# Kernel optimization log

Hardware: AMD Instinct MI355X
Metric: run time of the kernel (lower is better)

## Reference

```python
import jax, jax.numpy as jnp
import numpy as np

B, N, H, D = 4, 2048, 16, 64
FEATS = H * D  # 1024; module scales scores by sqrt(feats), not sqrt(head_dim)


def setup_inputs() -> dict:
    key = jax.random.key(0)
    ks = jax.random.split(key, 9)
    s = 1.0 / np.sqrt(D)
    return {
        "x": jax.random.normal(ks[0], (B, N, H, D), dtype=jnp.float32),
        "Wq": jax.random.uniform(ks[1], (H, D, D), jnp.float32, -s, s),
        "bq": jax.random.uniform(ks[2], (H, D), jnp.float32, -s, s),
        "Wk": jax.random.uniform(ks[3], (H, D, D), jnp.float32, -s, s),
        "bk": jax.random.uniform(ks[4], (H, D), jnp.float32, -s, s),
        "Wv": jax.random.uniform(ks[5], (H, D, D), jnp.float32, -s, s),
        "bv": jax.random.uniform(ks[6], (H, D), jnp.float32, -s, s),
        "Wo": jax.random.uniform(ks[7], (H, D, D), jnp.float32, -s, s),
        "bo": jax.random.uniform(ks[8], (H, D), jnp.float32, -s, s),
    }


def reference(x, Wq, bq, Wk, bk, Wv, bv, Wo, bo):
    # per-head linears as one batched einsum: [b,n,h,d] x [h,d,o] -> [b,n,h,o]
    q = jnp.einsum("bnhd,hdo->bnho", x, Wq) + bq
    k = jnp.einsum("bnhd,hdo->bnho", x, Wk) + bk
    v = jnp.einsum("bnhd,hdo->bnho", x, Wv) + bv
    sqrt_d = jnp.asarray(FEATS, x.dtype) ** 0.5  # sqrt(feats) per original code
    # scores: [b,h,i,j]
    score = jax.nn.softmax(jnp.einsum("bihf,bjhf->bhij", q, k) / sqrt_d, axis=-1)
    attn = jnp.einsum("bhij,bjhf->bihf", score, v)  # [b,n,h,d]
    out = jnp.einsum("bnhd,hdo->bnho", attn, Wo) + bo
    return out
```

## Files before the change

### kernel.cpp

```cpp
#include <hip/hip_runtime.h>

#define Bsz  4
#define Nseq 2048
#define Hn   16
#define Dh   64
#define BH   (Bsz*Hn)
#define NT64 (Nseq/64)
#define NT32 (Nseq/32)

#define AS1 __attribute__((address_space(1)))
#define AS3 __attribute__((address_space(3)))

typedef __attribute__((ext_vector_type(8))) short bf16x8;
typedef __attribute__((ext_vector_type(16))) float f32x16;
typedef __attribute__((ext_vector_type(4))) float f32x4;
typedef __attribute__((ext_vector_type(2))) float f32x2;
typedef __attribute__((ext_vector_type(4))) unsigned short u16x4;

#define MFMA32 __builtin_amdgcn_mfma_f32_32x32x16_bf16

static __device__ __forceinline__ unsigned short f2bf(float f) {
    unsigned u = __float_as_uint(f);
    u = (u + 0x7fffu + ((u >> 16) & 1u)) >> 16;
    return (unsigned short)u;
}
static __device__ __forceinline__ float bf2f(unsigned short s) {
    return __uint_as_float((unsigned)s << 16);
}
static __device__ __forceinline__ unsigned cvt_pk_bf16(float lo, float hi) {
    unsigned r;
    asm("v_cvt_pk_bf16_f32 %0, %1, %2" : "=v"(r) : "v"(lo), "v"(hi));
    return r;
}
static __device__ __forceinline__ void swap32(unsigned &a, unsigned &b) {
    asm("v_permlane32_swap_b32 %0, %1" : "+v"(a), "+v"(b));
}
static __device__ __forceinline__ float exp2v(float x) {
    float r;
    asm("v_exp_f32 %0, %1" : "=v"(r) : "v"(x));
    return r;
}
static __device__ __forceinline__ f32x2 pk_add(f32x2 a, f32x2 b) {
    f32x2 d;
    asm("v_pk_add_f32 %0, %1, %2" : "=v"(d) : "v"(a), "v"(b));
    return d;
}

__global__ __launch_bounds__(256) void wprep_kernel(
    const float* __restrict__ Wq, const float* __restrict__ Wk,
    const float* __restrict__ Wv,
    unsigned short* __restrict__ gWtH, unsigned short* __restrict__ gWtL)
{
    __shared__ float ws[64][65];
    const int mh = blockIdx.x;
    const int m = mh >> 4, h = mh & 15;
    const int tid = threadIdx.x;
    const float* W = (m == 0 ? Wq : (m == 1 ? Wk : Wv)) + h * 4096;

    for (int c = tid; c < 1024; c += 256) {
        int row = c >> 4, col = (c & 15) * 4;
        *(f32x4*)&ws[row][col] = *(const f32x4*)&W[row * 64 + col];
    }
    __syncthreads();

    const int o = tid >> 2, dblk = (tid & 3) * 16;
    size_t base = ((size_t)mh * 64 + o) * 64 + dblk;
#pragma unroll
    for (int i4 = 0; i4 < 4; ++i4) {
        u16x4 vh, vl;
#pragma unroll
        for (int j = 0; j < 4; ++j) {
            float v = ws[dblk + i4 * 4 + j][o];
            unsigned short hh = f2bf(v);
            vh[j] = hh;
            vl[j] = f2bf(v - bf2f(hh));
        }
        *(u16x4*)&gWtH[base + i4 * 4] = vh;
        *(u16x4*)&gWtL[base + i4 * 4] = vl;
    }
}

__global__ __launch_bounds__(256) void proj_kernel(
    const float* __restrict__ x,
    const unsigned short* __restrict__ gWtH, const unsigned short* __restrict__ gWtL,
    const float* __restrict__ bq, const float* __restrict__ bk,
    const float* __restrict__ bv,
    unsigned short* __restrict__ gQ, unsigned short* __restrict__ gK,
    unsigned short* __restrict__ gVt)
{
    __shared__ unsigned short st[64][72];

    const int bh = blockIdx.x, h = bh & (Hn - 1), b = bh >> 4;
    const int n0 = blockIdx.y * 64;
    const int tid = threadIdx.x;
    const int w = tid >> 6, lane = tid & 63, l31 = lane & 31, l5 = lane >> 5;
    const int qi = w >> 1, oj = w & 1;

    const int nrow = n0 + qi * 32 + l31;
    const float* xrow = x + (((size_t)b * Nseq + nrow) * Hn + h) * Dh;

    bf16x8 xh[4], xl[4];
#pragma unroll
    for (int ks = 0; ks < 4; ++ks) {
        f32x4 v0 = *(const f32x4*)&xrow[ks * 16 + l5 * 8];
        f32x4 v1 = *(const f32x4*)&xrow[ks * 16 + l5 * 8 + 4];
#pragma unroll
        for (int e = 0; e < 4; ++e) {
            unsigned short h0 = f2bf(v0[e]);
            xh[ks][e] = (short)h0;
            xl[ks][e] = (short)f2bf(v0[e] - bf2f(h0));
            unsigned short h1 = f2bf(v1[e]);
            xh[ks][4 + e] = (short)h1;
            xl[ks][4 + e] = (short)f2bf(v1[e] - bf2f(h1));
        }
    }

    const int o = oj * 32 + l31;

    f32x16 acc[3] = {};
#pragma unroll
    for (int m = 0; m < 3; ++m) {
        const unsigned short* WH = gWtH + (((size_t)m * 16 + h) * 64 + o) * 64;
        const unsigned short* WL = gWtL + (((size_t)m * 16 + h) * 64 + o) * 64;
#pragma unroll
        for (int ks = 0; ks < 4; ++ks) {
            bf16x8 wh = *(const bf16x8*)&WH[ks * 16 + l5 * 8];
            bf16x8 wl = *(const bf16x8*)&WL[ks * 16 + l5 * 8];
            if (m < 2) {
                acc[m] = MFMA32(xh[ks], wh, acc[m], 0, 0, 0);
                acc[m] = MFMA32(xl[ks], wh, acc[m], 0, 0, 0);
                acc[m] = MFMA32(xh[ks], wl, acc[m], 0, 0, 0);
            } else {
                acc[2] = MFMA32(wh, xh[ks], acc[2], 0, 0, 0);
                acc[2] = MFMA32(wl, xh[ks], acc[2], 0, 0, 0);
                acc[2] = MFMA32(wh, xl[ks], acc[2], 0, 0, 0);
            }
        }
    }

    const size_t gbase = (size_t)bh * Nseq + n0;

    {
        float bias = bq[h * 64 + o];
#pragma unroll
        for (int r = 0; r < 16; ++r) {
            int nl = (r & 3) + 8 * (r >> 2) + 4 * l5;
            st[qi * 32 + nl][o] = f2bf((acc[0][r] + bias) * 0.0450842200f);
        }
    }
    __syncthreads();
#pragma unroll
    for (int i = 0; i < 2; ++i) {
        int c = i * 256 + tid;
        int row = c >> 3, ch = c & 7;
        bf16x8 v = *(const bf16x8*)&st[row][ch * 8];
        *(bf16x8*)&gQ[(gbase + row) * Dh + ch * 8] = v;
    }
    __syncthreads();

    {
        float bias = bk[h * 64 + o];
#pragma unroll
        for (int r = 0; r < 16; ++r) {
            int nl = (r & 3) + 8 * (r >> 2) + 4 * l5;
            st[qi * 32 + nl][o] = f2bf(acc[1][r] + bias);
        }
    }
    __syncthreads();
#pragma unroll
    for (int i = 0; i < 2; ++i) {
        int c = i * 256 + tid;
        int row = c >> 3, ch = c & 7;
        bf16x8 v = *(const bf16x8*)&st[row][ch * 8];
        *(bf16x8*)&gK[(gbase + row) * Dh + ((ch ^ (row & 7)) * 8)] = v;
    }
    __syncthreads();

    {
#pragma unroll
        for (int r = 0; r < 16; ++r) {
            int ol = (r & 3) + 8 * (r >> 2) + 4 * l5;
            int ov = oj * 32 + ol;
            st[ov][qi * 32 + l31] = f2bf(acc[2][r] + bv[h * 64 + ov]);
        }
    }
    __syncthreads();
#pragma unroll
    for (int i = 0; i < 2; ++i) {
        int c = i * 256 + tid;
        int orow = c >> 3, ch = c & 7;
        int tile = ch >> 2, c4 = ch & 3;
        bf16x8 v = *(const bf16x8*)&st[orow][ch * 8];
        *(bf16x8*)&gVt[((size_t)(bh * NT32 + (n0 >> 5) + tile)) * 2048 +
                       orow * 32 + ((c4 ^ ((orow >> 2) & 3)) * 8)] = v;
    }
}

__global__ __launch_bounds__(256, 4) void flash_kernel(
    const unsigned short* __restrict__ gQ,
    const unsigned short* __restrict__ gK,
    const unsigned short* __restrict__ gVt,
    const float* __restrict__ Wo, const float* __restrict__ bo,
    float* __restrict__ out)
{
    __shared__ unsigned short kbuf[2][4096];
    __shared__ unsigned short vbuf[2][4096];

    const int bh = blockIdx.x, h = bh & (Hn - 1), b = bh >> 4;
    const int tid = threadIdx.x;
    const int w = tid >> 6, lane = tid & 63;
    const int l31 = lane & 31, l5 = lane >> 5;
    const int qrow = blockIdx.y * 128 + w * 32 + l31;

    bf16x8 qf[4];
#pragma unroll
    for (int kk = 0; kk < 4; ++kk)
        qf[kk] = *(const bf16x8*)&gQ[((size_t)bh * Nseq + qrow) * Dh + kk * 16 + l5 * 8];

    const unsigned short* kbase[4];
#pragma unroll
    for (int kk = 0; kk < 4; ++kk)
        kbase[kk] = &kbuf[0][l31 * 64 + (((kk * 2 + l5) ^ (l31 & 7)) * 8)];
    const unsigned short* vbase[2];
#pragma unroll
    for (int ks = 0; ks < 2; ++ks)
        vbase[ks] = &vbuf[0][l31 * 32 + (((ks * 2 + l5) ^ ((l31 >> 2) & 3)) * 8)];

    float z0 = 0.f;
    asm volatile("" : "+v"(z0));
    f32x16 zc = {z0, z0, z0, z0, z0, z0, z0, z0, z0, z0, z0, z0, z0, z0, z0, z0};

    f32x16 acc[2] = {};
    float l = 0.f;

    auto stage = [&](int t, int bufi) {
        const unsigned short* ks = gK + ((size_t)bh * Nseq + (size_t)t * 64) * Dh;
        const unsigned short* vs = gVt + ((size_t)(bh * NT32 + 2 * t)) * 2048;
#pragma unroll
        for (int i = 0; i < 2; ++i) {
            int off = w * 1024 + i * 512 + lane * 8;
            __builtin_amdgcn_global_load_lds((const AS1 void*)(ks + off),
                                             (AS3 void*)(&kbuf[bufi][w * 1024 + i * 512]), 16, 0, 0);
            __builtin_amdgcn_global_load_lds((const AS1 void*)(vs + off),
                                             (AS3 void*)(&vbuf[bufi][w * 1024 + i * 512]), 16, 0, 0);
        }
    };

    auto soft_pv = [&](f32x16& s, const int sub, const int buf) {
#pragma unroll
        for (int r = 0; r < 16; ++r) s[r] = exp2v(s[r]);
        f32x2* sp = (f32x2*)&s;
        f32x2 u0 = pk_add(sp[0], sp[1]), u1 = pk_add(sp[2], sp[3]);
        f32x2 u2 = pk_add(sp[4], sp[5]), u3 = pk_add(sp[6], sp[7]);
        u0 = pk_add(u0, u1); u2 = pk_add(u2, u3);
        u0 = pk_add(u0, u2);
        l += u0[0] + u0[1];
#pragma unroll
        for (int ks = 0; ks < 2; ++ks) {
            const int b0 = 8 * ks;
            unsigned x0 = cvt_pk_bf16(s[b0 + 0], s[b0 + 1]);
            unsigned x1 = cvt_pk_bf16(s[b0 + 2], s[b0 + 3]);
            unsigned y0 = cvt_pk_bf16(s[b0 + 4], s[b0 + 5]);
            unsigned y1 = cvt_pk_bf16(s[b0 + 6], s[b0 + 7]);
            swap32(x0, y0);
            swap32(x1, y1);
            bf16x8 pf;
            ((unsigned*)&pf)[0] = x0; ((unsigned*)&pf)[1] = x1;
            ((unsigned*)&pf)[2] = y0; ((unsigned*)&pf)[3] = y1;
            __builtin_amdgcn_s_setprio(1);
#pragma unroll
            for (int dt = 0; dt < 2; ++dt) {
                bf16x8 vf = *(const bf16x8*)(vbase[ks] + dt * 1024 + sub * 2048 + buf * 4096);
                acc[dt] = MFMA32(vf, pf, acc[dt], 0, 0, 0);
            }
            __builtin_amdgcn_s_setprio(0);
        }
    };

    auto window = [&](const int buf) {
        f32x16 sA, sB;
        __builtin_amdgcn_s_setprio(1);
        {
            bf16x8 kf = *(const bf16x8*)(kbase[0] + buf * 4096);
            sA = MFMA32(kf, qf[0], zc, 0, 0, 0);
            kf = *(const bf16x8*)(kbase[1] + buf * 4096);
            sA = MFMA32(kf, qf[1], sA, 0, 0, 0);
            kf = *(const bf16x8*)(kbase[2] + buf * 4096);
            sA = MFMA32(kf, qf[2], sA, 0, 0, 0);
            kf = *(const bf16x8*)(kbase[3] + buf * 4096);
            sA = MFMA32(kf, qf[3], sA, 0, 0, 0);
            kf = *(const bf16x8*)(kbase[0] + 2048 + buf * 4096);
            sB = MFMA32(kf, qf[0], zc, 0, 0, 0);
            kf = *(const bf16x8*)(kbase[1] + 2048 + buf * 4096);
            sB = MFMA32(kf, qf[1], sB, 0, 0, 0);
            kf = *(const bf16x8*)(kbase[2] + 2048 + buf * 4096);
            sB = MFMA32(kf, qf[2], sB, 0, 0, 0);
            kf = *(const bf16x8*)(kbase[3] + 2048 + buf * 4096);
            sB = MFMA32(kf, qf[3], sB, 0, 0, 0);
        }
        __builtin_amdgcn_s_setprio(0);
        soft_pv(sA, 0, buf);
        soft_pv(sB, 1, buf);
    };

    stage(0, 0);

#pragma unroll 1
    for (int t2 = 0; t2 < NT64; t2 += 2) {
        __syncthreads();
        stage(t2 + 1, 1);
        window(0);
        __syncthreads();
        if (t2 + 2 < NT64) stage(t2 + 2, 0);
        window(1);
    }

    __syncthreads();
    {
        unsigned short* wl = &kbuf[0][0];
        for (int c = tid; c < 512; c += 256) {
            int o = c >> 3, c8 = c & 7;
            int cc = ((c8 ^ (o & 7)) * 8);
#pragma unroll
            for (int jj = 0; jj < 4; ++jj) wl[o * 64 + cc + jj]     = f2bf(Wo[(h * 64 + c8 * 8 + jj) * 64 + o]);
#pragma unroll
            for (int jj = 0; jj < 4; ++jj) wl[o * 64 + cc + 4 + jj] = f2bf(Wo[(h * 64 + c8 * 8 + 4 + jj) * 64 + o]);
        }
    }
    __syncthreads();

    l += __shfl_xor(l, 32);
    float inv = 1.f / l;
#pragma unroll
    for (int dt = 0; dt < 2; ++dt)
#pragma unroll
        for (int r = 0; r < 16; ++r) acc[dt][r] *= inv;

    f32x16 oc[2] = {};
#pragma unroll
    for (int kk = 0; kk < 4; ++kk) {
        const int dt = kk >> 1;
        const int b0 = 8 * (kk & 1);
        unsigned x0 = cvt_pk_bf16(acc[dt][b0 + 0], acc[dt][b0 + 1]);
        unsigned x1 = cvt_pk_bf16(acc[dt][b0 + 2], acc[dt][b0 + 3]);
        unsigned y0 = cvt_pk_bf16(acc[dt][b0 + 4], acc[dt][b0 + 5]);
        unsigned y1 = cvt_pk_bf16(acc[dt][b0 + 6], acc[dt][b0 + 7]);
        swap32(x0, y0);
        swap32(x1, y1);
        bf16x8 af;
        ((unsigned*)&af)[0] = x0; ((unsigned*)&af)[1] = x1;
        ((unsigned*)&af)[2] = y0; ((unsigned*)&af)[3] = y1;
#pragma unroll
        for (int ot = 0; ot < 2; ++ot) {
            bf16x8 wf = *(const bf16x8*)(kbase[kk] + ot * 2048);
            oc[ot] = MFMA32(wf, af, oc[ot], 0, 0, 0);
        }
    }

    float* obase = out + (((size_t)b * Nseq + qrow) * Hn + h) * Dh;
#pragma unroll
    for (int ot = 0; ot < 2; ++ot)
#pragma unroll
        for (int rq = 0; rq < 4; ++rq) {
            int o = ot * 32 + rq * 8 + l5 * 4;
            f32x4 bb = *(const f32x4*)&bo[h * 64 + o];
            f32x4 vv;
            vv[0] = oc[ot][rq * 4 + 0] + bb[0];
            vv[1] = oc[ot][rq * 4 + 1] + bb[1];
            vv[2] = oc[ot][rq * 4 + 2] + bb[2];
            vv[3] = oc[ot][rq * 4 + 3] + bb[3];
            *(f32x4*)&obase[o] = vv;
        }
}

extern "C" void kernel_launch(void* const* d_in, const int* in_sizes, int n_in,
                              void* d_out, int out_size, void* d_ws, size_t ws_size,
                              hipStream_t stream) {
    const float* x  = (const float*)d_in[0];
    const float* Wq = (const float*)d_in[1];
    const float* bq = (const float*)d_in[2];
    const float* Wk = (const float*)d_in[3];
    const float* bk = (const float*)d_in[4];
    const float* Wv = (const float*)d_in[5];
    const float* bv = (const float*)d_in[6];
    const float* Wo = (const float*)d_in[7];
    const float* bo = (const float*)d_in[8];
    float* out = (float*)d_out;

    unsigned short* gQ   = (unsigned short*)d_ws;
    unsigned short* gK   = gQ + (size_t)BH * Nseq * Dh;
    unsigned short* gVt  = gK + (size_t)BH * Nseq * Dh;
    unsigned short* gWtH = gVt + (size_t)BH * Nseq * Dh;
    unsigned short* gWtL = gWtH + (size_t)3 * 16 * 64 * 64;

    wprep_kernel<<<48, 256, 0, stream>>>(Wq, Wk, Wv, gWtH, gWtL);
    proj_kernel<<<dim3(BH, Nseq / 64), 256, 0, stream>>>(x, gWtH, gWtL, bq, bk, bv, gQ, gK, gVt);
    flash_kernel<<<dim3(BH, Nseq / 128), 256, 0, stream>>>(gQ, gK, gVt, Wo, bo, out);
}
```

Measured before the change: 130.3 us.

## Software-pipeline QK of next tile with softmax/PV of current tile

Restructures the flash attention main loop so the QK^T MFMAs for tile t+1 are issued alongside the exp/softmax and PV work for tile t. K now uses a 4-slot LDS ring and V stays double-buffered, which allows one barrier per tile instead of two. The setprio hints are removed. LDS use rises, launch bounds drop from 4 to 3 blocks per CU, and the final iteration computes one redundant clamped QK tile.

```diff
diff --git a/kernel.cpp b/kernel.cpp
--- a/kernel.cpp
+++ b/kernel.cpp
@@ -196,14 +196,14 @@
     }
 }
 
-__global__ __launch_bounds__(256, 4) void flash_kernel(
+__global__ __launch_bounds__(256, 3) void flash_kernel(
     const unsigned short* __restrict__ gQ,
     const unsigned short* __restrict__ gK,
     const unsigned short* __restrict__ gVt,
     const float* __restrict__ Wo, const float* __restrict__ bo,
     float* __restrict__ out)
 {
-    __shared__ unsigned short kbuf[2][4096];
+    __shared__ unsigned short kbuf[4][4096];
     __shared__ unsigned short vbuf[2][4096];
 
     const int bh = blockIdx.x, h = bh & (Hn - 1), b = bh >> 4;
@@ -233,20 +233,39 @@
     f32x16 acc[2] = {};
     float l = 0.f;
 
-    auto stage = [&](int t, int bufi) {
+    auto stageK = [&](int t, int slot) {
         const unsigned short* ks = gK + ((size_t)bh * Nseq + (size_t)t * 64) * Dh;
-        const unsigned short* vs = gVt + ((size_t)(bh * NT32 + 2 * t)) * 2048;
 #pragma unroll
         for (int i = 0; i < 2; ++i) {
             int off = w * 1024 + i * 512 + lane * 8;
             __builtin_amdgcn_global_load_lds((const AS1 void*)(ks + off),
-                                             (AS3 void*)(&kbuf[bufi][w * 1024 + i * 512]), 16, 0, 0);
+                                             (AS3 void*)(&kbuf[slot][w * 1024 + i * 512]), 16, 0, 0);
+        }
+    };
+    auto stageV = [&](int t, int slot) {
+        const unsigned short* vs = gVt + ((size_t)(bh * NT32 + 2 * t)) * 2048;
+#pragma unroll
+        for (int i = 0; i < 2; ++i) {
+            int off = w * 1024 + i * 512 + lane * 8;
             __builtin_amdgcn_global_load_lds((const AS1 void*)(vs + off),
-                                             (AS3 void*)(&vbuf[bufi][w * 1024 + i * 512]), 16, 0, 0);
+                                             (AS3 void*)(&vbuf[slot][w * 1024 + i * 512]), 16, 0, 0);
         }
     };
 
-    auto soft_pv = [&](f32x16& s, const int sub, const int buf) {
+    auto qk_sub = [&](const int slot, const int sub) -> f32x16 {
+        const int o = slot * 4096 + sub * 2048;
+        bf16x8 kf = *(const bf16x8*)(kbase[0] + o);
+        f32x16 s = MFMA32(kf, qf[0], zc, 0, 0, 0);
+        kf = *(const bf16x8*)(kbase[1] + o);
+        s = MFMA32(kf, qf[1], s, 0, 0, 0);
+        kf = *(const bf16x8*)(kbase[2] + o);
+        s = MFMA32(kf, qf[2], s, 0, 0, 0);
+        kf = *(const bf16x8*)(kbase[3] + o);
+        s = MFMA32(kf, qf[3], s, 0, 0, 0);
+        return s;
+    };
+
+    auto soft_pv = [&](f32x16& s, const int sub, const int vslot) {
 #pragma unroll
         for (int r = 0; r < 16; ++r) s[r] = exp2v(s[r]);
         f32x2* sp = (f32x2*)&s;
@@ -267,55 +286,37 @@
             bf16x8 pf;
             ((unsigned*)&pf)[0] = x0; ((unsigned*)&pf)[1] = x1;
             ((unsigned*)&pf)[2] = y0; ((unsigned*)&pf)[3] = y1;
-            __builtin_amdgcn_s_setprio(1);
 #pragma unroll
             for (int dt = 0; dt < 2; ++dt) {
-                bf16x8 vf = *(const bf16x8*)(vbase[ks] + dt * 1024 + sub * 2048 + buf * 4096);
+                bf16x8 vf = *(const bf16x8*)(vbase[ks] + dt * 1024 + sub * 2048 + vslot * 4096);
                 acc[dt] = MFMA32(vf, pf, acc[dt], 0, 0, 0);
             }
-            __builtin_amdgcn_s_setprio(0);
         }
     };
 
-    auto window = [&](const int buf) {
-        f32x16 sA, sB;
-        __builtin_amdgcn_s_setprio(1);
-        {
-            bf16x8 kf = *(const bf16x8*)(kbase[0] + buf * 4096);
-            sA = MFMA32(kf, qf[0], zc, 0, 0, 0);
-            kf = *(const bf16x8*)(kbase[1] + buf * 4096);
-            sA = MFMA32(kf, qf[1], sA, 0, 0, 0);
-            kf = *(const bf16x8*)(kbase[2] + buf * 4096);
-            sA = MFMA32(kf, qf[2], sA, 0, 0, 0);
-            kf = *(const bf16x8*)(kbase[3] + buf * 4096);
-            sA = MFMA32(kf, qf[3], sA, 0, 0, 0);
-            kf = *(const bf16x8*)(kbase[0] + 2048 + buf * 4096);
-            sB = MFMA32(kf, qf[0], zc, 0, 0, 0);
-            kf = *(const bf16x8*)(kbase[1] + 2048 + buf * 4096);
-            sB = MFMA32(kf, qf[1], sB, 0, 0, 0);
-            kf = *(const bf16x8*)(kbase[2] + 2048 + buf * 4096);
-            sB = MFMA32(kf, qf[2], sB, 0, 0, 0);
-            kf = *(const bf16x8*)(kbase[3] + 2048 + buf * 4096);
-            sB = MFMA32(kf, qf[3], sB, 0, 0, 0);
-        }
-        __builtin_amdgcn_s_setprio(0);
-        soft_pv(sA, 0, buf);
-        soft_pv(sB, 1, buf);
-    };
-
-    stage(0, 0);
+    stageK(0, 0);
+    stageV(0, 0);
+    stageK(1, 1);
+    __syncthreads();
+    f32x16 sA = qk_sub(0, 0);
+    f32x16 sB = qk_sub(0, 1);
 
 #pragma unroll 1
-    for (int t2 = 0; t2 < NT64; t2 += 2) {
-        __syncthreads();
-        stage(t2 + 1, 1);
-        window(0);
-        __syncthreads();
-        if (t2 + 2 < NT64) stage(t2 + 2, 0);
-        window(1);
-    }
-
-    __syncthreads();
+    for (int t4 = 0; t4 < NT64; t4 += 4) {
+#pragma unroll
+        for (int u = 0; u < 4; ++u) {
+            const int t = t4 + u;
+            stageK(min(t + 2, NT64 - 1), (u + 2) & 3);
+            stageV(min(t + 1, NT64 - 1), (u + 1) & 1);
+            f32x16 nA = qk_sub((u + 1) & 3, 0);
+            soft_pv(sA, 0, u & 1);
+            f32x16 nB = qk_sub((u + 1) & 3, 1);
+            soft_pv(sB, 1, u & 1);
+            sA = nA; sB = nB;
+            __syncthreads();
+        }
+    }
+
     {
         unsigned short* wl = &kbuf[0][0];
         for (int c = tid; c < 512; c += 256) {
```

Measured after the change: 133.5 us. 2.5% more time.
